# Performance work log

Hardware: AMD Instinct MI355X
Metric: run time of the kernel (lower is better)

## Reference

```python
import jax, jax.numpy as jnp
import numpy as np

N_NODES = 50000
N_EDGES = 800000
F_IN = 64
F_HID = 64
K = 3


def _cheb_norm(edge_index, edge_weight, n):
    # PyG ChebConv sym normalization with lambda_max=2: Lhat = -D^{-1/2} A D^{-1/2}
    # (diagonal of Lhat is exactly 0, so self-loop terms vanish)
    row, col = edge_index[0], edge_index[1]
    deg = jax.ops.segment_sum(edge_weight, row, num_segments=n)
    dis = jnp.where(deg > 0, jax.lax.rsqrt(jnp.where(deg > 0, deg, 1.0)), 0.0)
    return -dis[row] * edge_weight * dis[col]


def _prop(x, row, col, norm, n):
    # out[i] = sum_{e: col[e]=i} norm[e] * x[row[e]]
    return jax.ops.segment_sum(x[row] * norm[:, None], col, num_segments=n)


def _cheb_conv(x, W, b, row, col, norm, n):
    # ChebConv K=3: Tx0=x, Tx1=Lhat x, Tx2=2 Lhat Tx1 - Tx0
    tx0 = x
    tx1 = _prop(x, row, col, norm, n)
    tx2 = 2.0 * _prop(tx1, row, col, norm, n) - tx0
    return tx0 @ W[0] + tx1 @ W[1] + tx2 @ W[2] + b


def setup_inputs() -> dict:
    key = jax.random.key(0)
    ks = jax.random.split(key, 20)
    inp = {
        "x": jax.random.normal(ks[0], (N_NODES, F_IN), dtype=jnp.float32),
        "edge_index": jax.random.randint(ks[1], (2, N_EDGES), 0, N_NODES, dtype=jnp.int32),
        "edge_weight": jax.random.uniform(ks[2], (N_EDGES,), dtype=jnp.float32),
    }
    # 6 ChebConvs: x->gate (F_IN->F_HID) and h->gate (F_HID->F_HID) for z, r, h
    names_in = [("Wxz", "bxz", F_IN), ("Whz", "bhz", F_HID), ("Wxr", "bxr", F_IN),
                ("Whr", "bhr", F_HID), ("Wxh", "bxh", F_IN), ("Whh", "bhh", F_HID)]
    for i, (wn, bn, fin) in enumerate(names_in):
        scale = 1.0 / np.sqrt(fin)
        inp[wn] = jax.random.normal(ks[3 + i], (K, fin, F_HID), dtype=jnp.float32) * scale
        inp[bn] = jnp.zeros((F_HID,), dtype=jnp.float32)
    inp["Wlin"] = jax.random.normal(ks[12], (F_HID, 2), dtype=jnp.float32) * (1.0 / np.sqrt(F_HID))
    inp["blin"] = jnp.zeros((2,), dtype=jnp.float32)
    return inp


def reference(x, edge_index, edge_weight, Wxz, bxz, Whz, bhz, Wxr, bxr, Whr, bhr,
              Wxh, bxh, Whh, bhh, Wlin, blin):
    n = x.shape[0]
    row, col = edge_index[0], edge_index[1]
    norm = _cheb_norm(edge_index, edge_weight, n)
    h0 = jnp.zeros((n, F_HID), dtype=x.dtype)
    # GConvGRU single step (initial hidden state = 0)
    z = jax.nn.sigmoid(_cheb_conv(x, Wxz, bxz, row, col, norm, n)
                       + _cheb_conv(h0, Whz, bhz, row, col, norm, n))
    r = jax.nn.sigmoid(_cheb_conv(x, Wxr, bxr, row, col, norm, n)
                       + _cheb_conv(h0, Whr, bhr, row, col, norm, n))
    h_tilde = jnp.tanh(_cheb_conv(x, Wxh, bxh, row, col, norm, n)
                       + _cheb_conv(h0 * r, Whh, bhh, row, col, norm, n))
    h = z * h0 + (1.0 - z) * h_tilde
    # head: dropout in eval mode (identity) -> tanh -> linear -> sigmoid
    return jax.nn.sigmoid(jnp.tanh(h) @ Wlin + blin)
```

## Files before the change

### kernel.cpp

```cpp
#include <hip/hip_runtime.h>
#include <hip/hip_bf16.h>

#define N_NODES 50000
#define N_EDGES 800000
#define NB1 400
#define CH  2000
#define NBKT 196
#define CAP 8192
#define SORT_MAX 6144

typedef unsigned short ushort_t;
typedef unsigned long long u64;
typedef __attribute__((ext_vector_type(8))) short bf16x8;
typedef __attribute__((ext_vector_type(4))) float f32x4;

constexpr int GCUR_O  = 0;
constexpr int DIS_O   = 512;
constexpr int OFF_O   = 50512;
constexpr int CSLOT_O = 100544;
constexpr int RSLOT_O = 3311808;
constexpr int RW_O    = 4917440;
constexpr int ABUF_O  = 6517440;
constexpr int PBUF_O  = 11317440;
constexpr int XS_O    = 11329728;
constexpr int T1S_O   = RSLOT_O;

__device__ __forceinline__ ushort_t f32_to_bf16(float f) {
    unsigned u = __float_as_uint(f);
    u += 0x7fffu + ((u >> 16) & 1u);
    return (ushort_t)(u >> 16);
}
__device__ __forceinline__ float bflo(unsigned u) { return __uint_as_float(u << 16); }
__device__ __forceinline__ float bfhi(unsigned u) { return __uint_as_float(u & 0xffff0000u); }
__device__ __forceinline__ unsigned packbf2(float a, float b) {
    return (unsigned)f32_to_bf16(a) | ((unsigned)f32_to_bf16(b) << 16);
}
__device__ __forceinline__ float fsigmoid(float x) { return 1.f / (1.f + __expf(-x)); }
__device__ __forceinline__ float ftanh(float x) {
    x = fminf(15.f, fmaxf(-15.f, x));
    float e = __expf(2.f * x);
    return (e - 1.f) / (e + 1.f);
}

__device__ __forceinline__ unsigned block_scan256_incl(unsigned v, int t, unsigned* wsum) {
    int lane = t & 63;
    unsigned sc = v;
#pragma unroll
    for (int o = 1; o < 64; o <<= 1) {
        unsigned u = __shfl_up(sc, o, 64);
        if (lane >= o) sc += u;
    }
    if (t < 256 && lane == 63) wsum[t >> 6] = sc;
    __syncthreads();
    if (t < 256) {
        int wid = t >> 6;
        unsigned off = 0;
#pragma unroll
        for (int wv = 0; wv < 3; ++wv) if (wv < wid) off += wsum[wv];
        sc += off;
    }
    __syncthreads();
    return sc;
}

__global__ __launch_bounds__(512) void k1(
    const int* __restrict__ ei, const float* __restrict__ ew,
    const float* __restrict__ Wxz, const float* __restrict__ Wxh,
    unsigned* __restrict__ gcur, u64* __restrict__ cslot,
    unsigned* __restrict__ rslot, ushort_t* __restrict__ pbuf) {
    int bid = blockIdx.x, t = threadIdx.x;
    __shared__ u64 pC[CH];
    __shared__ ushort_t ordC[CH], ordR[CH];
    __shared__ unsigned char digC[CH], digR[CH];
    __shared__ unsigned hc[256], hr[256], scC[256], scR[256], bc[256], br[256];
    __shared__ unsigned wsum[8];
    if (bid < NB1) {
        if (t < 256) { hc[t] = 0; hr[t] = 0; }
        __syncthreads();
        int e0 = bid * CH;
        for (int i = t; i < CH; i += 512) {
            unsigned r = (unsigned)ei[e0 + i];
            unsigned c = (unsigned)ei[N_EDGES + e0 + i];
            unsigned w = __float_as_uint(ew[e0 + i]);
            unsigned dc = c >> 8;
            pC[i] = ((u64)w << 32) | (dc << 24) | ((c & 255u) << 16) | (r & 0xFFFFu);
            atomicAdd(&hc[dc], 1u);
            atomicAdd(&hr[r >> 8], 1u);
        }
        __syncthreads();
        if (t < NBKT) {
            bc[t] = atomicAdd(&gcur[t], hc[t]);
            br[t] = atomicAdd(&gcur[256 + t], hr[t]);
        }
        unsigned vC = (t < 256) ? hc[t] : 0u;
        unsigned vR = (t < 256) ? hr[t] : 0u;
        unsigned iC = block_scan256_incl(vC, t, wsum);
        unsigned iR = block_scan256_incl(vR, t, wsum);
        if (t < 256) {
            scC[t] = iC - vC;
            scR[t] = iR - vR;
            hc[t] = 0; hr[t] = 0;
        }
        __syncthreads();
        for (int i = t; i < CH; i += 512) {
            u64 p = pC[i];
            unsigned dc = (unsigned)(p >> 24) & 255u;
            unsigned pc = scC[dc] + atomicAdd(&hc[dc], 1u);
            ordC[pc] = (ushort_t)i;
            digC[pc] = (unsigned char)dc;
            unsigned r = (unsigned)p & 0xFFFFu;
            unsigned dr = r >> 8;
            unsigned pr = scR[dr] + atomicAdd(&hr[dr], 1u);
            ordR[pr] = (ushort_t)i;
            digR[pr] = (unsigned char)dr;
        }
        __syncthreads();
        for (int i = t; i < CH; i += 512) {
            unsigned dc = digC[i];
            u64 p = pC[ordC[i]];
            unsigned slotC = bc[dc] + (unsigned)i - scC[dc];
            if (slotC < CAP) cslot[(size_t)dc * CAP + slotC] = p;
            unsigned dr = digR[i];
            u64 q = pC[ordR[i]];
            unsigned slotR = br[dr] + (unsigned)i - scR[dr];
            if (slotR < CAP)
                rslot[(size_t)dr * CAP + slotR] =
                    ((unsigned)(q >> 32) & 0xFFFFFF00u) | ((unsigned)q & 255u);
        }
    } else {
        for (int idx = t; idx < 24576; idx += 512) {
            int k = idx >> 7, n = idx & 127;
            float v = (n < 64) ? Wxz[k * 64 + n] : Wxh[k * 64 + (n - 64)];
            int c = n >> 4, s = k >> 5, l = (((k >> 3) & 3) << 4) | (n & 15), j = k & 7;
            pbuf[((c * 6 + s) * 64 + l) * 8 + j] = f32_to_bf16(v);
        }
    }
}

__global__ __launch_bounds__(512) void k2(
    const float* __restrict__ x, const unsigned* __restrict__ gcur,
    const u64* __restrict__ cslot, const unsigned* __restrict__ rslot,
    float* __restrict__ dis, int* __restrict__ off, u64* __restrict__ rw,
    unsigned* __restrict__ abuf, unsigned* __restrict__ xs) {
    int bid = blockIdx.x, t = threadIdx.x;
    __shared__ u64 srt[SORT_MAX];
    __shared__ unsigned hist[256], hsc[256], cur[256], gs[256];
    __shared__ unsigned wsum[8];
    __shared__ float facc[256];

    if (bid < NBKT) {
        unsigned szv = (t < NBKT) ? gcur[t] : 0u;
        unsigned inc = block_scan256_incl(szv, t, wsum);
        if (t < 256) gs[t] = inc - szv;
        if (t < 256) hist[t] = 0;
        __syncthreads();
        unsigned szb = gcur[bid];
        unsigned sz = min(szb, (unsigned)SORT_MAX);
        unsigned base = gs[bid];
        const u64* cs = cslot + (size_t)bid * CAP;
        for (unsigned i = t; i < sz; i += 512)
            atomicAdd(&hist[((unsigned)cs[i] >> 16) & 255u], 1u);
        __syncthreads();
        unsigned h0 = (t < 256) ? hist[t] : 0u;
        unsigned hinc = block_scan256_incl(h0, t, wsum);
        if (t < 256) {
            hsc[t] = hinc - h0;
            cur[t] = 0u;
            int c = bid * 256 + t;
            if (c <= N_NODES) off[c] = (int)(base + hsc[t]);
        }
        __syncthreads();
        for (unsigned i = t; i < sz; i += 512) {
            u64 v = cs[i];
            unsigned d = ((unsigned)v >> 16) & 255u;
            unsigned p = hsc[d] + atomicAdd(&cur[d], 1u);
            srt[p] = v;
        }
        __syncthreads();
        for (unsigned i = t; i < sz; i += 512) {
            u64 v = srt[i];
            rw[base + i] = ((v >> 32) << 32) | ((unsigned)v & 0xFFFFu);
        }
    } else {
        int b = bid - NBKT;
        if (t < 256) facc[t] = 0.f;
        __syncthreads();
        unsigned szr = min(gcur[256 + b], (unsigned)CAP);
        const unsigned* rs = rslot + (size_t)b * CAP;
        for (unsigned i = t; i < szr; i += 512)
            atomicAdd(&facc[rs[i] & 255u], __uint_as_float(rs[i] & 0xFFFFFF00u));
        __syncthreads();
        if (t < 256) {
            float d = facc[t];
            float r = d > 0.f ? rsqrtf(d) : 0.f;
            facc[t] = r;
            int n = b * 256 + t;
            if (n < N_NODES) dis[n] = r;
        }
        __syncthreads();
        for (int idx = t; idx < 8192; idx += 512) {
            int nl = idx >> 5, q = idx & 31;
            int n = b * 256 + nl;
            if (n < N_NODES) {
                float2 xv = ((const float2*)x)[n * 32 + q];
                float r = facc[nl];
                abuf[n * 96 + q] = packbf2(xv.x, xv.y);
                xs[n * 32 + q] = packbf2(r * xv.x, r * xv.y);
            }
        }
    }
}

__global__ __launch_bounds__(256) void k_prop(
    const int* __restrict__ off, const u64* __restrict__ rw,
    const unsigned* __restrict__ xsrc, const float* __restrict__ dis,
    const float* __restrict__ xf, unsigned* __restrict__ abuf,
    unsigned* __restrict__ t1s, int mode) {
    int node = (blockIdx.x * 256 + threadIdx.x) >> 6;
    if (node >= N_NODES) return;
    int lane = threadIdx.x & 63, h = lane >> 5, q = lane & 31;
    int b = off[node], end = off[node + 1];
    float di = dis[node];
    float acc0 = 0.f, acc1 = 0.f;
    for (; b + 7 < end; b += 8) {
        u64 v0 = rw[b + h], v1 = rw[b + h + 2], v2 = rw[b + h + 4], v3 = rw[b + h + 6];
        unsigned u0 = xsrc[((unsigned)v0 & 0xFFFFu) * 32 + q];
        unsigned u1 = xsrc[((unsigned)v1 & 0xFFFFu) * 32 + q];
        unsigned u2 = xsrc[((unsigned)v2 & 0xFFFFu) * 32 + q];
        unsigned u3 = xsrc[((unsigned)v3 & 0xFFFFu) * 32 + q];
        float a0 = __uint_as_float((unsigned)(v0 >> 32));
        float a1 = __uint_as_float((unsigned)(v1 >> 32));
        float a2 = __uint_as_float((unsigned)(v2 >> 32));
        float a3 = __uint_as_float((unsigned)(v3 >> 32));
        acc0 += a0 * bflo(u0) + a1 * bflo(u1) + a2 * bflo(u2) + a3 * bflo(u3);
        acc1 += a0 * bfhi(u0) + a1 * bfhi(u1) + a2 * bfhi(u2) + a3 * bfhi(u3);
    }
    for (; b + 1 < end; b += 2) {
        u64 v = rw[b + h];
        unsigned u = xsrc[((unsigned)v & 0xFFFFu) * 32 + q];
        float a = __uint_as_float((unsigned)(v >> 32));
        acc0 += a * bflo(u); acc1 += a * bfhi(u);
    }
    if (b < end && h == 0) {
        u64 v = rw[b];
        unsigned u = xsrc[((unsigned)v & 0xFFFFu) * 32 + q];
        float a = __uint_as_float((unsigned)(v >> 32));
        acc0 += a * bflo(u); acc1 += a * bfhi(u);
    }
    acc0 += __shfl_xor(acc0, 32, 64);
    acc1 += __shfl_xor(acc1, 32, 64);
    if (h == 0) {
        float t0 = -di * acc0, t1v = -di * acc1;
        if (mode == 0) {
            abuf[node * 96 + 32 + q] = packbf2(t0, t1v);
            t1s[node * 32 + q] = packbf2(di * t0, di * t1v);
        } else {
            float2 xv = ((const float2*)xf)[node * 32 + q];
            abuf[node * 96 + 64 + q] = packbf2(2.f * t0 - xv.x, 2.f * t1v - xv.y);
        }
    }
}

__global__ __launch_bounds__(256) void k_gemm(
    const ushort_t* __restrict__ ab, const ushort_t* __restrict__ pbuf,
    const float* __restrict__ bxz, const float* __restrict__ bhz,
    const float* __restrict__ bxh, const float* __restrict__ bhh,
    const float* __restrict__ Wlin, const float* __restrict__ blin,
    float2* __restrict__ out) {
    __shared__ ushort_t bsh[24576];
    int tid = threadIdx.x;
    {
        uint4* s4 = (uint4*)bsh;
        const uint4* g4 = (const uint4*)pbuf;
        for (int i = tid; i < 3072; i += 256) s4[i] = g4[i];
    }
    __syncthreads();

    int wave = tid >> 6, lane = tid & 63;
    int quad = lane >> 4, m = lane & 15;

    float bzv[4], bhv[4], wl0[4], wl1[4];
#pragma unroll
    for (int c = 0; c < 4; ++c) {
        int col = c * 16 + m;
        bzv[c] = bxz[col] + bhz[col];
        bhv[c] = bxh[col] + bhh[col];
        wl0[c] = Wlin[2 * col];
        wl1[c] = Wlin[2 * col + 1];
    }
    float bl0 = blin[0], bl1 = blin[1];

    for (int tile = 0; tile < 2; ++tile) {
        int n0 = (blockIdx.x * 2 + tile) * 64;
        int arow = n0 + wave * 16 + m;
        const ushort_t* ap = ab + (size_t)arow * 192 + quad * 8;

        f32x4 acc[8];
#pragma unroll
        for (int c = 0; c < 8; ++c) acc[c] = (f32x4){0.f, 0.f, 0.f, 0.f};
#pragma unroll
        for (int s = 0; s < 6; ++s) {
            bf16x8 af = *(const bf16x8*)(ap + s * 32);
#pragma unroll
            for (int c = 0; c < 8; ++c) {
                bf16x8 bfr = *(const bf16x8*)(bsh + ((c * 6 + s) * 64 + lane) * 8);
                acc[c] = __builtin_amdgcn_mfma_f32_16x16x32_bf16(af, bfr, acc[c], 0, 0, 0);
            }
        }
#pragma unroll
        for (int i = 0; i < 4; ++i) {
            float p0 = 0.f, p1 = 0.f;
#pragma unroll
            for (int c = 0; c < 4; ++c) {
                float z  = fsigmoid(acc[c][i] + bzv[c]);
                float ht = ftanh(acc[c + 4][i] + bhv[c]);
                float t  = ftanh((1.f - z) * ht);
                p0 += t * wl0[c];
                p1 += t * wl1[c];
            }
            for (int o = 1; o <= 8; o <<= 1) {
                p0 += __shfl_xor(p0, o, 64);
                p1 += __shfl_xor(p1, o, 64);
            }
            int g = n0 + wave * 16 + quad * 4 + i;
            if (m == 0 && g < N_NODES)
                out[g] = make_float2(fsigmoid(p0 + bl0), fsigmoid(p1 + bl1));
        }
    }
}

extern "C" void kernel_launch(void* const* d_in, const int* in_sizes, int n_in,
                              void* d_out, int out_size, void* d_ws, size_t ws_size,
                              hipStream_t stream) {
    const float* x    = (const float*)d_in[0];
    const int*   ei   = (const int*)d_in[1];
    const float* ew   = (const float*)d_in[2];
    const float* Wxz  = (const float*)d_in[3];
    const float* bxz  = (const float*)d_in[4];
    const float* bhz  = (const float*)d_in[6];
    const float* Wxh  = (const float*)d_in[11];
    const float* bxh  = (const float*)d_in[12];
    const float* bhh  = (const float*)d_in[14];
    const float* Wlin = (const float*)d_in[15];
    const float* blin = (const float*)d_in[16];

    float*    ws    = (float*)d_ws;
    unsigned* gcur  = (unsigned*)(ws + GCUR_O);
    float*    dis   = ws + DIS_O;
    int*      off   = (int*)(ws + OFF_O);
    u64*      cslot = (u64*)(ws + CSLOT_O);
    unsigned* rslot = (unsigned*)(ws + RSLOT_O);
    u64*      rw    = (u64*)(ws + RW_O);
    unsigned* abuf  = (unsigned*)(ws + ABUF_O);
    ushort_t* pbuf  = (ushort_t*)(ws + PBUF_O);
    unsigned* xs    = (unsigned*)(ws + XS_O);
    unsigned* t1s   = (unsigned*)(ws + T1S_O);

    hipMemsetAsync(d_ws, 0, 512 * 4, stream);

    k1<<<NB1 + 1, 512, 0, stream>>>(ei, ew, Wxz, Wxh, gcur, cslot, rslot, pbuf);
    k2<<<NBKT * 2, 512, 0, stream>>>(x, gcur, cslot, rslot, dis, off, rw, abuf, xs);
    k_prop<<<12500, 256, 0, stream>>>(off, rw, xs, dis, x, abuf, t1s, 0);
    k_prop<<<12500, 256, 0, stream>>>(off, rw, t1s, dis, x, abuf, abuf, 1);
    k_gemm<<<391, 256, 0, stream>>>((const ushort_t*)abuf, pbuf, bxz, bhz, bxh, bhh,
                                    Wlin, blin, (float2*)d_out);
}
```

Measured before the change: 209.1 us.

## Split k2 bucket sort and degree blocks into half-buckets; double k1 blocks

Each k2 bucket is now handled by two blocks, each owning one half of the 256 destination slots. Both blocks still read the whole bucket and build the full histogram, but each scatters and writes only its own half. The degree/normalisation blocks are split the same way, and k1 now launches twice as many blocks with half the chunk size. The aim is more parallelism across CUs for these setup kernels, at the cost of every bucket being read twice and the histogram work being duplicated.

After: 225.2 us. +7.7%, slower.

```diff
diff --git a/kernel.cpp b/kernel.cpp
--- a/kernel.cpp
+++ b/kernel.cpp
@@ -3,8 +3,8 @@
 
 #define N_NODES 50000
 #define N_EDGES 800000
-#define NB1 400
-#define CH  2000
+#define NB1 800
+#define CH  1000
 #define NBKT 196
 #define CAP 8192
 #define SORT_MAX 6144
@@ -146,18 +146,19 @@
     __shared__ u64 srt[SORT_MAX];
     __shared__ unsigned hist[256], hsc[256], cur[256], gs[256];
     __shared__ unsigned wsum[8];
-    __shared__ float facc[256];
-
-    if (bid < NBKT) {
+    __shared__ float facc[128];
+
+    if (bid < 2 * NBKT) {
+        int b = bid >> 1, hf = bid & 1;
         unsigned szv = (t < NBKT) ? gcur[t] : 0u;
         unsigned inc = block_scan256_incl(szv, t, wsum);
         if (t < 256) gs[t] = inc - szv;
         if (t < 256) hist[t] = 0;
         __syncthreads();
-        unsigned szb = gcur[bid];
-        unsigned sz = min(szb, (unsigned)SORT_MAX);
-        unsigned base = gs[bid];
-        const u64* cs = cslot + (size_t)bid * CAP;
+        unsigned szb = gcur[b];
+        unsigned sz = min(szb, (unsigned)CAP);
+        unsigned base = gs[b];
+        const u64* cs = cslot + (size_t)b * CAP;
         for (unsigned i = t; i < sz; i += 512)
             atomicAdd(&hist[((unsigned)cs[i] >> 16) & 255u], 1u);
         __syncthreads();
@@ -166,41 +167,56 @@
         if (t < 256) {
             hsc[t] = hinc - h0;
             cur[t] = 0u;
-            int c = bid * 256 + t;
-            if (c <= N_NODES) off[c] = (int)(base + hsc[t]);
+        }
+        __syncthreads();
+        unsigned startHalf = hsc[hf * 128];
+        unsigned endHalf = hf ? sz : hsc[128];
+        if (t < 128) {
+            int d = hf * 128 + t;
+            int c = b * 256 + d;
+            if (c <= N_NODES) off[c] = (int)(base + hsc[d]);
         }
         __syncthreads();
         for (unsigned i = t; i < sz; i += 512) {
             u64 v = cs[i];
             unsigned d = ((unsigned)v >> 16) & 255u;
-            unsigned p = hsc[d] + atomicAdd(&cur[d], 1u);
-            srt[p] = v;
-        }
-        __syncthreads();
-        for (unsigned i = t; i < sz; i += 512) {
+            if ((d >> 7) == (unsigned)hf) {
+                unsigned p = hsc[d] - startHalf + atomicAdd(&cur[d], 1u);
+                if (p < (unsigned)SORT_MAX) srt[p] = v;
+            }
+        }
+        __syncthreads();
+        unsigned szHalf = min(endHalf - startHalf, (unsigned)SORT_MAX);
+        for (unsigned i = t; i < szHalf; i += 512) {
             u64 v = srt[i];
-            rw[base + i] = ((v >> 32) << 32) | ((unsigned)v & 0xFFFFu);
+            rw[base + startHalf + i] = ((v >> 32) << 32) | ((unsigned)v & 0xFFFFu);
         }
     } else {
-        int b = bid - NBKT;
-        if (t < 256) facc[t] = 0.f;
+        int idx2 = bid - 2 * NBKT;
+        int b = idx2 >> 1, hf = idx2 & 1;
+        if (t < 128) facc[t] = 0.f;
         __syncthreads();
         unsigned szr = min(gcur[256 + b], (unsigned)CAP);
         const unsigned* rs = rslot + (size_t)b * CAP;
-        for (unsigned i = t; i < szr; i += 512)
-            atomicAdd(&facc[rs[i] & 255u], __uint_as_float(rs[i] & 0xFFFFFF00u));
-        __syncthreads();
-        if (t < 256) {
+        for (unsigned i = t; i < szr; i += 512) {
+            unsigned v = rs[i];
+            unsigned r8 = v & 255u;
+            if ((r8 >> 7) == (unsigned)hf)
+                atomicAdd(&facc[r8 & 127u], __uint_as_float(v & 0xFFFFFF00u));
+        }
+        __syncthreads();
+        int nbase = b * 256 + hf * 128;
+        if (t < 128) {
             float d = facc[t];
             float r = d > 0.f ? rsqrtf(d) : 0.f;
             facc[t] = r;
-            int n = b * 256 + t;
+            int n = nbase + t;
             if (n < N_NODES) dis[n] = r;
         }
         __syncthreads();
-        for (int idx = t; idx < 8192; idx += 512) {
+        for (int idx = t; idx < 4096; idx += 512) {
             int nl = idx >> 5, q = idx & 31;
-            int n = b * 256 + nl;
+            int n = nbase + nl;
             if (n < N_NODES) {
                 float2 xv = ((const float2*)x)[n * 32 + q];
                 float r = facc[nl];
@@ -359,7 +375,7 @@
     hipMemsetAsync(d_ws, 0, 512 * 4, stream);
 
     k1<<<NB1 + 1, 512, 0, stream>>>(ei, ew, Wxz, Wxh, gcur, cslot, rslot, pbuf);
-    k2<<<NBKT * 2, 512, 0, stream>>>(x, gcur, cslot, rslot, dis, off, rw, abuf, xs);
+    k2<<<4 * NBKT, 512, 0, stream>>>(x, gcur, cslot, rslot, dis, off, rw, abuf, xs);
     k_prop<<<12500, 256, 0, stream>>>(off, rw, xs, dis, x, abuf, t1s, 0);
     k_prop<<<12500, 256, 0, stream>>>(off, rw, t1s, dis, x, abuf, abuf, 1);
     k_gemm<<<391, 256, 0, stream>>>((const ushort_t*)abuf, pbuf, bxz, bhz, bxh, bhh,
```
